# Kernel tuning notes

Hardware: AMD Instinct MI355X
Metric: run time of the kernel (lower is better)

The kernel has to match this reference:

```python
import jax, jax.numpy as jnp
import numpy as np

N = 20000          # nodes
F = 256            # num_node_features (== num_sampled_vectors)
FEAT_EMB = 63      # feat_emb_dim
EMB = FEAT_EMB + 1 # emb_dim = feat_emb_dim + val_emb_dim
CH = F * EMB       # 16384, conv1 input channels
HID = 128
OUT = 7
E = 320000         # edges


def setup_inputs() -> dict:
    key = jax.random.key(0)
    ks = jax.random.split(key, 7)
    x = jax.random.normal(ks[0], (N, F), dtype=jnp.float32)
    emb_table = jax.random.normal(ks[1], (F, FEAT_EMB), dtype=jnp.float32) * 0.02
    W1 = jax.random.normal(ks[2], (CH, HID), dtype=jnp.float32) / np.sqrt(CH)
    b1 = jnp.zeros((HID,), jnp.float32)
    W2 = jax.random.normal(ks[3], (HID, OUT), dtype=jnp.float32) / np.sqrt(HID)
    b2 = jnp.zeros((OUT,), jnp.float32)
    edge_index = jax.random.randint(ks[4], (2, E), 0, N, dtype=jnp.int32)
    return {"x": x, "emb_table": emb_table, "W1": W1, "b1": b1,
            "W2": W2, "b2": b2, "edge_index": edge_index}


def _gcn_conv(h, W, b, src, dst, norm, n):
    # PyG GCNConv: symmetric-normalized aggregation (with self loops) of x @ W, then + bias
    h = h @ W                                   # [n, out]
    msg = h[src] * norm[:, None]                # gather + edge-weight
    agg = jax.ops.segment_sum(msg, dst, num_segments=n)  # scatter-add
    return agg + b


def reference(x, emb_table, W1, b1, W2, b2, edge_index):
    n = x.shape[0]
    # StandardScaler: per-feature zero mean, unit (population) std
    mean = x.mean(axis=0)
    std = x.std(axis=0)
    std = jnp.where(std == 0, jnp.float32(1.0), std)
    xs = (x - mean) / std                       # [n, F]
    # feature embedding construction: per node, concat emb_table with its value column
    feats = jnp.concatenate(
        [jnp.broadcast_to(emb_table[None], (n, F, FEAT_EMB)), xs[:, :, None]],
        axis=-1,
    ).reshape(n, CH)                            # [n, F*EMB]
    # GCN normalization with self loops (eval mode: no dropout_adj / dropout)
    loop = jnp.arange(n, dtype=edge_index.dtype)
    src = jnp.concatenate([edge_index[0], loop])
    dst = jnp.concatenate([edge_index[1], loop])
    deg = jax.ops.segment_sum(jnp.ones_like(src, jnp.float32), dst, num_segments=n)
    dinv = jnp.where(deg > 0, jax.lax.rsqrt(deg), jnp.float32(0.0))
    norm = dinv[src] * dinv[dst]                # [E+n]
    h = jax.nn.relu(_gcn_conv(feats, W1, b1, src, dst, norm, n))
    out = _gcn_conv(h, W2, b2, src, dst, norm, n)
    return jax.nn.log_softmax(out, axis=1)
```

## Files before the change

### kernel.cpp

```cpp
#include <hip/hip_runtime.h>
#include <math.h>

#define F_   256
#define FEAT_EMB_ 63
#define HID_ 128
#define OUT_ 7
#define SLOTS 64
#define NP 16

typedef short short8 __attribute__((ext_vector_type(8)));
typedef float f32x4 __attribute__((ext_vector_type(4)));

__device__ inline short f2bf(float f) {
    unsigned u = __float_as_uint(f);
    u += 0x7FFFu + ((u >> 16) & 1u);
    return (short)(u >> 16);
}

#define K1_CS 625
#define K1_ED 625
#define K1_CV 256
#define K1_PK 16
#define K1_GRID (K1_CS + K1_ED + K1_CV + K1_PK)

__global__ __launch_bounds__(256) void k1_kernel(const float* __restrict__ x,
                                                 const int* __restrict__ ei,
                                                 const float* __restrict__ emb,
                                                 const float* __restrict__ W1,
                                                 float* __restrict__ colsum16,
                                                 float* __restrict__ colsq16,
                                                 int* __restrict__ deg,
                                                 int* __restrict__ adjP,
                                                 float* __restrict__ Cp16,
                                                 short* __restrict__ Wfrag, int E) {
    __shared__ float4 smem[8 * 64];
    int b = blockIdx.x;
    int t = threadIdx.x;

    if (b < K1_CS) {
        int rl = t >> 6, lane = t & 63;
        int row0 = b * 32 + rl * 8;
        float4 v[8];
#pragma unroll
        for (int i = 0; i < 8; i++)
            v[i] = *(const float4*)(x + (size_t)(row0 + i) * F_ + lane * 4);
        float4 s = make_float4(0.f, 0.f, 0.f, 0.f);
        float4 q = make_float4(0.f, 0.f, 0.f, 0.f);
#pragma unroll
        for (int i = 0; i < 8; i++) {
            s.x += v[i].x; s.y += v[i].y; s.z += v[i].z; s.w += v[i].w;
            q.x += v[i].x * v[i].x; q.y += v[i].y * v[i].y;
            q.z += v[i].z * v[i].z; q.w += v[i].w * v[i].w;
        }
        smem[rl * 64 + lane] = s;
        smem[(rl + 4) * 64 + lane] = q;
        __syncthreads();
        if (rl == 0) {
#pragma unroll
            for (int i = 1; i < 4; i++) {
                float4 a = smem[i * 64 + lane], bq = smem[(i + 4) * 64 + lane];
                s.x += a.x; s.y += a.y; s.z += a.z; s.w += a.w;
                q.x += bq.x; q.y += bq.y; q.z += bq.z; q.w += bq.w;
            }
            int buf = (b & (NP - 1)) * F_;
            atomicAdd(&colsum16[buf + lane * 4 + 0], s.x);
            atomicAdd(&colsum16[buf + lane * 4 + 1], s.y);
            atomicAdd(&colsum16[buf + lane * 4 + 2], s.z);
            atomicAdd(&colsum16[buf + lane * 4 + 3], s.w);
            atomicAdd(&colsq16[buf + lane * 4 + 0], q.x);
            atomicAdd(&colsq16[buf + lane * 4 + 1], q.y);
            atomicAdd(&colsq16[buf + lane * 4 + 2], q.z);
            atomicAdd(&colsq16[buf + lane * 4 + 3], q.w);
        }
    } else if (b < K1_CS + K1_ED) {
        int e0 = (b - K1_CS) * 512 + t;
#pragma unroll
        for (int i = 0; i < 2; i++) {
            int e = e0 + i * 256;
            if (e < E) {
                int s = ei[e];
                int d = ei[E + e];
                int pos = atomicAdd(&deg[d], 1);
                if (pos < SLOTS) adjP[(d << 6) + pos] = s;
            }
        }
    } else if (b < K1_CS + K1_ED + K1_CV) {
        int f = b - (K1_CS + K1_ED);
        int jg = t >> 5, k4 = t & 31;
        float4 s = make_float4(0.f, 0.f, 0.f, 0.f);
        for (int j = jg; j < FEAT_EMB_; j += 8) {
            float e = emb[f * FEAT_EMB_ + j];
            float4 w = *(const float4*)(W1 + ((size_t)(f * 64 + j)) * HID_ + k4 * 4);
            s.x += e * w.x; s.y += e * w.y; s.z += e * w.z; s.w += e * w.w;
        }
        smem[jg * 32 + k4] = s;
        __syncthreads();
        if (jg == 0) {
#pragma unroll
            for (int i = 1; i < 8; i++) {
                float4 a = smem[i * 32 + k4];
                s.x += a.x; s.y += a.y; s.z += a.z; s.w += a.w;
            }
            int buf = (f & (NP - 1)) * HID_;
            atomicAdd(&Cp16[buf + k4 * 4 + 0], s.x);
            atomicAdd(&Cp16[buf + k4 * 4 + 1], s.y);
            atomicAdd(&Cp16[buf + k4 * 4 + 2], s.z);
            atomicAdd(&Cp16[buf + k4 * 4 + 3], s.w);
        }
    } else {
        int pb = b - (K1_CS + K1_ED + K1_CV);
        int f0 = pb * 16;
#pragma unroll
        for (int i = 0; i < 8; i++) {
            int idx = t + i * 256;
            int f = f0 + (idx >> 7);
            int nn = idx & 127;
            float w = W1[((size_t)(f * 64 + 63)) * HID_ + nn];
            int kc = f >> 5, j = f & 7, hi2 = (f >> 3) & 3;
            int lane = hi2 * 16 + (nn & 15);
            int nt = nn >> 4;
            Wfrag[(((kc * 8 + nt) * 64 + lane) << 3) + j] = f2bf(w);
        }
    }
}

__global__ __launch_bounds__(256) void mm1_kernel(const float* __restrict__ x,
                                                  const short* __restrict__ Wfrag,
                                                  const float* __restrict__ Cp16,
                                                  const float* __restrict__ colsum16,
                                                  const float* __restrict__ colsq16,
                                                  const int* __restrict__ deg,
                                                  unsigned short* __restrict__ g0b,
                                                  int n) {
    __shared__ float cps[HID_];
    __shared__ float smean[F_];
    __shared__ float srstd[F_];
    int t = threadIdx.x;
    {
        float s = 0.f, q = 0.f;
#pragma unroll
        for (int p = 0; p < NP; p++) {
            s += colsum16[p * F_ + t];
            q += colsq16[p * F_ + t];
        }
        float m = s / (float)n;
        float var = fmaxf(q / (float)n - m * m, 0.f);
        float sd = sqrtf(var);
        smean[t] = m;
        srstd[t] = (sd == 0.f) ? 1.f : (1.f / sd);
    }
    if (t < HID_) {
        float s = 0.f;
#pragma unroll
        for (int p = 0; p < NP; p++) s += Cp16[p * HID_ + t];
        cps[t] = s;
    }
    __syncthreads();

    int wave = t >> 6, lane = t & 63;
    int m = lane & 15;
    int hi = lane >> 4;
    int rowbase = blockIdx.x * 64 + wave * 16;
    int arow = rowbase + m;
    bool rok = arow < n;
    const float* xrow = x + (size_t)arow * F_ + hi * 8;

    float4 xa[8], xb[8];
    if (rok) {
#pragma unroll
        for (int kc = 0; kc < 8; kc++) {
            xa[kc] = *(const float4*)(xrow + kc * 32);
            xb[kc] = *(const float4*)(xrow + kc * 32 + 4);
        }
    }

    const float4* smv = (const float4*)smean;
    const float4* srv = (const float4*)srstd;

    f32x4 acc[8];
#pragma unroll
    for (int i = 0; i < 8; i++) acc[i] = (f32x4){0.f, 0.f, 0.f, 0.f};

#pragma unroll
    for (int kc = 0; kc < 8; kc++) {
        short8 af;
        if (rok) {
            int mb = kc * 8 + hi * 2;
            float4 m0 = smv[mb], m1 = smv[mb + 1];
            float4 r0 = srv[mb], r1 = srv[mb + 1];
            af[0] = f2bf((xa[kc].x - m0.x) * r0.x);
            af[1] = f2bf((xa[kc].y - m0.y) * r0.y);
            af[2] = f2bf((xa[kc].z - m0.z) * r0.z);
            af[3] = f2bf((xa[kc].w - m0.w) * r0.w);
            af[4] = f2bf((xb[kc].x - m1.x) * r1.x);
            af[5] = f2bf((xb[kc].y - m1.y) * r1.y);
            af[6] = f2bf((xb[kc].z - m1.z) * r1.z);
            af[7] = f2bf((xb[kc].w - m1.w) * r1.w);
        } else {
            af = (short8){0, 0, 0, 0, 0, 0, 0, 0};
        }
#pragma unroll
        for (int nt = 0; nt < 8; nt++) {
            short8 bf = *(const short8*)(Wfrag + (((kc * 8 + nt) * 64 + lane) << 3));
            acc[nt] = __builtin_amdgcn_mfma_f32_16x16x32_bf16(af, bf, acc[nt], 0, 0, 0);
        }
    }

    float dv[4];
#pragma unroll
    for (int r = 0; r < 4; r++) {
        int gr = rowbase + hi * 4 + r;
        dv[r] = (gr < n) ? rsqrtf((float)deg[gr] + 1.0f) : 0.f;
    }
#pragma unroll
    for (int nt = 0; nt < 8; nt++) {
        int col = nt * 16 + m;
        float cp = cps[col];
#pragma unroll
        for (int r = 0; r < 4; r++) {
            int gr = rowbase + hi * 4 + r;
            if (gr < n)
                g0b[(size_t)gr * HID_ + col] = (unsigned short)f2bf((acc[nt][r] + cp) * dv[r]);
        }
    }
}

__global__ __launch_bounds__(256) void agg_fc2_kernel(const unsigned short* __restrict__ g0b,
                                                      const int* __restrict__ deg,
                                                      const int* __restrict__ adjP,
                                                      const float* __restrict__ b1,
                                                      const float* __restrict__ W2,
                                                      float* __restrict__ g2, int n) {
    int wave = threadIdx.x >> 6;
    int lane = threadIdx.x & 63;
    int d = blockIdx.x * 4 + wave;
    if (d >= n) return;

    int dgv = deg[d];
    int o0 = d << 6;
    int o1 = o0 + min(dgv, SLOTS);
    unsigned u = *(const unsigned*)(g0b + (size_t)d * HID_ + lane * 2);
    float ax = __uint_as_float(u << 16);
    float ay = __uint_as_float(u & 0xFFFF0000u);

    for (int base = o0; base < o1; base += 64) {
        int idx = (base + lane < o1) ? adjP[base + lane] : 0;
        int c2 = min(64, o1 - base);
        int j = 0;
        for (; j + 4 <= c2; j += 4) {
            int s0 = __shfl(idx, j + 0);
            int s1 = __shfl(idx, j + 1);
            int s2 = __shfl(idx, j + 2);
            int s3 = __shfl(idx, j + 3);
            unsigned u0 = *(const unsigned*)(g0b + (size_t)s0 * HID_ + lane * 2);
            unsigned u1 = *(const unsigned*)(g0b + (size_t)s1 * HID_ + lane * 2);
            unsigned u2 = *(const unsigned*)(g0b + (size_t)s2 * HID_ + lane * 2);
            unsigned u3 = *(const unsigned*)(g0b + (size_t)s3 * HID_ + lane * 2);
            ax += __uint_as_float(u0 << 16) + __uint_as_float(u1 << 16)
                + __uint_as_float(u2 << 16) + __uint_as_float(u3 << 16);
            ay += __uint_as_float(u0 & 0xFFFF0000u) + __uint_as_float(u1 & 0xFFFF0000u)
                + __uint_as_float(u2 & 0xFFFF0000u) + __uint_as_float(u3 & 0xFFFF0000u);
        }
        for (; j < c2; j++) {
            int s = __shfl(idx, j);
            unsigned uu = *(const unsigned*)(g0b + (size_t)s * HID_ + lane * 2);
            ax += __uint_as_float(uu << 16);
            ay += __uint_as_float(uu & 0xFFFF0000u);
        }
    }

    float dv = rsqrtf((float)dgv + 1.0f);
    float2 bb = *(const float2*)(b1 + lane * 2);
    float h0 = fmaxf(ax * dv + bb.x, 0.f);
    float h1 = fmaxf(ay * dv + bb.y, 0.f);

    const float* w2a = W2 + (lane * 2) * OUT_;
    const float* w2b = W2 + (lane * 2 + 1) * OUT_;
    float r[OUT_];
#pragma unroll
    for (int c = 0; c < OUT_; c++) {
        float p = h0 * w2a[c] + h1 * w2b[c];
#pragma unroll
        for (int off = 32; off > 0; off >>= 1) p += __shfl_xor(p, off);
        r[c] = p;
    }
    if (lane < 8) {
        float val;
        switch (lane) {
            case 0: val = r[0]; break;
            case 1: val = r[1]; break;
            case 2: val = r[2]; break;
            case 3: val = r[3]; break;
            case 4: val = r[4]; break;
            case 5: val = r[5]; break;
            case 6: val = r[6]; break;
            default: val = 0.f; break;
        }
        g2[(size_t)d * 8 + lane] = val * dv;
    }
}

__global__ __launch_bounds__(256) void agg2_softmax_kernel(const float* __restrict__ g2,
                                                           const int* __restrict__ deg,
                                                           const int* __restrict__ adjP,
                                                           const float* __restrict__ b2,
                                                           float* __restrict__ out, int n) {
    int t = threadIdx.x;
    int g = t >> 3;
    int c = t & 7;
    int d = blockIdx.x * 32 + g;
    if (d >= n) return;

    int dgv = deg[d];
    int o0 = d << 6;
    int o1 = o0 + min(dgv, SLOTS);
    float acc = g2[(size_t)d * 8 + c];
    int i = o0;
    for (; i + 2 <= o1; i += 2) {
        int s0 = adjP[i], s1 = adjP[i + 1];
        acc += g2[(size_t)s0 * 8 + c] + g2[(size_t)s1 * 8 + c];
    }
    for (; i < o1; i++) acc += g2[(size_t)adjP[i] * 8 + c];

    float dv = rsqrtf((float)dgv + 1.0f);
    float z = (c < OUT_) ? (acc * dv + b2[c]) : -INFINITY;
    float m = z;
#pragma unroll
    for (int off = 4; off > 0; off >>= 1) m = fmaxf(m, __shfl_xor(m, off, 8));
    float e = (c < OUT_) ? __expf(z - m) : 0.f;
    float sum = e;
#pragma unroll
    for (int off = 4; off > 0; off >>= 1) sum += __shfl_xor(sum, off, 8);
    if (c < OUT_) out[(size_t)d * OUT_ + c] = z - m - __logf(sum);
}

extern "C" void kernel_launch(void* const* d_in, const int* in_sizes, int n_in,
                              void* d_out, int out_size, void* d_ws, size_t ws_size,
                              hipStream_t stream) {
    const float* x    = (const float*)d_in[0];
    const float* emb  = (const float*)d_in[1];
    const float* W1   = (const float*)d_in[2];
    const float* b1   = (const float*)d_in[3];
    const float* W2   = (const float*)d_in[4];
    const float* b2   = (const float*)d_in[5];
    const int*   ei   = (const int*)d_in[6];
    float* out = (float*)d_out;

    const int N = in_sizes[0] / F_;
    const int E = in_sizes[6] / 2;

    float* ws = (float*)d_ws;
    size_t o = 0;
    float* colsum16 = ws + o; o += NP * F_;
    float* colsq16  = ws + o; o += NP * F_;
    float* Cp16     = ws + o; o += NP * HID_;
    int*   deg      = (int*)(ws + o); o += N;
    size_t zero_elems = o;
    short* Wfrag    = (short*)(ws + o); o += (size_t)F_ * HID_ / 2;
    int*   adjP     = (int*)(ws + o); o += (size_t)N * SLOTS;
    unsigned short* g0b = (unsigned short*)(ws + o); o += (size_t)N * HID_ / 2;
    float* g2       = ws + o; o += (size_t)N * 8;

    hipMemsetAsync(ws, 0, zero_elems * sizeof(float), stream);
    k1_kernel<<<K1_GRID, 256, 0, stream>>>(x, ei, emb, W1, colsum16, colsq16,
                                           deg, adjP, Cp16, Wfrag, E);
    mm1_kernel<<<(N + 63) / 64, 256, 0, stream>>>(x, Wfrag, Cp16, colsum16, colsq16,
                                                  deg, g0b, N);
    agg_fc2_kernel<<<(N + 3) / 4, 256, 0, stream>>>(g0b, deg, adjP, b1, W2, g2, N);
    agg2_softmax_kernel<<<(N + 31) / 32, 256, 0, stream>>>(g2, deg, adjP, b2, out, N);
}
```

Baseline: 147.7 us.

## Fold standardization into W1 fragments in shared memory, widen aggregation loops

The per-feature mean and std scaling moves into the weight side. Each mm1 block now builds a bf16 W1 fragment scaled by rstd in LDS (64KB) and adds a bias correction of -mean*w into the constant term. This removes the separate packing blocks in k1 and the per-element normalization of x, at the cost of every mm1 block reading and converting the W1 value columns redundantly. It also raises occupancy pressure from the larger LDS footprint. Separately, the first aggregation unrolls its gather by 8 instead of 4, and the second aggregation splits each node's neighbour list across two half-groups that are combined with a shuffle.

```diff
diff --git a/kernel.cpp b/kernel.cpp
--- a/kernel.cpp
+++ b/kernel.cpp
@@ -20,8 +20,7 @@
 #define K1_CS 625
 #define K1_ED 625
 #define K1_CV 256
-#define K1_PK 16
-#define K1_GRID (K1_CS + K1_ED + K1_CV + K1_PK)
+#define K1_GRID (K1_CS + K1_ED + K1_CV)
 
 __global__ __launch_bounds__(256) void k1_kernel(const float* __restrict__ x,
                                                  const int* __restrict__ ei,
@@ -32,7 +31,7 @@
                                                  int* __restrict__ deg,
                                                  int* __restrict__ adjP,
                                                  float* __restrict__ Cp16,
-                                                 short* __restrict__ Wfrag, int E) {
+                                                 int E) {
     __shared__ float4 smem[8 * 64];
     int b = blockIdx.x;
     int t = threadIdx.x;
@@ -84,7 +83,7 @@
                 if (pos < SLOTS) adjP[(d << 6) + pos] = s;
             }
         }
-    } else if (b < K1_CS + K1_ED + K1_CV) {
+    } else {
         int f = b - (K1_CS + K1_ED);
         int jg = t >> 5, k4 = t & 31;
         float4 s = make_float4(0.f, 0.f, 0.f, 0.f);
@@ -107,35 +106,23 @@
             atomicAdd(&Cp16[buf + k4 * 4 + 2], s.z);
             atomicAdd(&Cp16[buf + k4 * 4 + 3], s.w);
         }
-    } else {
-        int pb = b - (K1_CS + K1_ED + K1_CV);
-        int f0 = pb * 16;
-#pragma unroll
-        for (int i = 0; i < 8; i++) {
-            int idx = t + i * 256;
-            int f = f0 + (idx >> 7);
-            int nn = idx & 127;
-            float w = W1[((size_t)(f * 64 + 63)) * HID_ + nn];
-            int kc = f >> 5, j = f & 7, hi2 = (f >> 3) & 3;
-            int lane = hi2 * 16 + (nn & 15);
-            int nt = nn >> 4;
-            Wfrag[(((kc * 8 + nt) * 64 + lane) << 3) + j] = f2bf(w);
-        }
     }
 }
 
 __global__ __launch_bounds__(256) void mm1_kernel(const float* __restrict__ x,
-                                                  const short* __restrict__ Wfrag,
-                                                  const float* __restrict__ Cp16,
+                                                  const float* __restrict__ W1,
                                                   const float* __restrict__ colsum16,
                                                   const float* __restrict__ colsq16,
+                                                  const float* __restrict__ Cp16,
                                                   const int* __restrict__ deg,
                                                   unsigned short* __restrict__ g0b,
                                                   int n) {
+    __shared__ short wfrag[F_ * HID_];
+    __shared__ float smean[F_], srstd[F_];
+    __shared__ float red[256];
     __shared__ float cps[HID_];
-    __shared__ float smean[F_];
-    __shared__ float srstd[F_];
     int t = threadIdx.x;
+
     {
         float s = 0.f, q = 0.f;
 #pragma unroll
@@ -149,11 +136,31 @@
         smean[t] = m;
         srstd[t] = (sd == 0.f) ? 1.f : (1.f / sd);
     }
+    __syncthreads();
+
+    {
+        int nn = t & 127;
+        int f0 = t >> 7;
+        float cacc = 0.f;
+#pragma unroll
+        for (int i = 0; i < 128; i++) {
+            int f = f0 + i * 2;
+            float w = W1[((size_t)(f * 64 + 63)) * HID_ + nn];
+            float wr = w * srstd[f];
+            cacc -= smean[f] * wr;
+            int kc = f >> 5, j = f & 7, hi2 = (f >> 3) & 3;
+            int lane = hi2 * 16 + (nn & 15);
+            int nt = nn >> 4;
+            wfrag[(((kc * 8 + nt) * 64 + lane) << 3) + j] = f2bf(wr);
+        }
+        red[t] = cacc;
+    }
+    __syncthreads();
     if (t < HID_) {
-        float s = 0.f;
-#pragma unroll
-        for (int p = 0; p < NP; p++) s += Cp16[p * HID_ + t];
-        cps[t] = s;
+        float cv = 0.f;
+#pragma unroll
+        for (int p = 0; p < NP; p++) cv += Cp16[p * HID_ + t];
+        cps[t] = cv + red[t] + red[t + 128];
     }
     __syncthreads();
 
@@ -165,17 +172,26 @@
     bool rok = arow < n;
     const float* xrow = x + (size_t)arow * F_ + hi * 8;
 
-    float4 xa[8], xb[8];
+    short8 af[8];
     if (rok) {
+        float4 xa[8], xb[8];
 #pragma unroll
         for (int kc = 0; kc < 8; kc++) {
             xa[kc] = *(const float4*)(xrow + kc * 32);
             xb[kc] = *(const float4*)(xrow + kc * 32 + 4);
         }
-    }
-
-    const float4* smv = (const float4*)smean;
-    const float4* srv = (const float4*)srstd;
+#pragma unroll
+        for (int kc = 0; kc < 8; kc++) {
+            af[kc][0] = f2bf(xa[kc].x); af[kc][1] = f2bf(xa[kc].y);
+            af[kc][2] = f2bf(xa[kc].z); af[kc][3] = f2bf(xa[kc].w);
+            af[kc][4] = f2bf(xb[kc].x); af[kc][5] = f2bf(xb[kc].y);
+            af[kc][6] = f2bf(xb[kc].z); af[kc][7] = f2bf(xb[kc].w);
+        }
+    } else {
+#pragma unroll
+        for (int kc = 0; kc < 8; kc++)
+            af[kc] = (short8){0, 0, 0, 0, 0, 0, 0, 0};
+    }
 
     f32x4 acc[8];
 #pragma unroll
@@ -183,26 +199,10 @@
 
 #pragma unroll
     for (int kc = 0; kc < 8; kc++) {
-        short8 af;
-        if (rok) {
-            int mb = kc * 8 + hi * 2;
-            float4 m0 = smv[mb], m1 = smv[mb + 1];
-            float4 r0 = srv[mb], r1 = srv[mb + 1];
-            af[0] = f2bf((xa[kc].x - m0.x) * r0.x);
-            af[1] = f2bf((xa[kc].y - m0.y) * r0.y);
-            af[2] = f2bf((xa[kc].z - m0.z) * r0.z);
-            af[3] = f2bf((xa[kc].w - m0.w) * r0.w);
-            af[4] = f2bf((xb[kc].x - m1.x) * r1.x);
-            af[5] = f2bf((xb[kc].y - m1.y) * r1.y);
-            af[6] = f2bf((xb[kc].z - m1.z) * r1.z);
-            af[7] = f2bf((xb[kc].w - m1.w) * r1.w);
-        } else {
-            af = (short8){0, 0, 0, 0, 0, 0, 0, 0};
-        }
 #pragma unroll
         for (int nt = 0; nt < 8; nt++) {
-            short8 bf = *(const short8*)(Wfrag + (((kc * 8 + nt) * 64 + lane) << 3));
-            acc[nt] = __builtin_amdgcn_mfma_f32_16x16x32_bf16(af, bf, acc[nt], 0, 0, 0);
+            short8 bf = *(const short8*)(wfrag + (((kc * 8 + nt) * 64 + lane) << 3));
+            acc[nt] = __builtin_amdgcn_mfma_f32_16x16x32_bf16(af[kc], bf, acc[nt], 0, 0, 0);
         }
     }
 
@@ -247,19 +247,18 @@
         int idx = (base + lane < o1) ? adjP[base + lane] : 0;
         int c2 = min(64, o1 - base);
         int j = 0;
-        for (; j + 4 <= c2; j += 4) {
-            int s0 = __shfl(idx, j + 0);
-            int s1 = __shfl(idx, j + 1);
-            int s2 = __shfl(idx, j + 2);
-            int s3 = __shfl(idx, j + 3);
-            unsigned u0 = *(const unsigned*)(g0b + (size_t)s0 * HID_ + lane * 2);
-            unsigned u1 = *(const unsigned*)(g0b + (size_t)s1 * HID_ + lane * 2);
-            unsigned u2 = *(const unsigned*)(g0b + (size_t)s2 * HID_ + lane * 2);
-            unsigned u3 = *(const unsigned*)(g0b + (size_t)s3 * HID_ + lane * 2);
-            ax += __uint_as_float(u0 << 16) + __uint_as_float(u1 << 16)
-                + __uint_as_float(u2 << 16) + __uint_as_float(u3 << 16);
-            ay += __uint_as_float(u0 & 0xFFFF0000u) + __uint_as_float(u1 & 0xFFFF0000u)
-                + __uint_as_float(u2 & 0xFFFF0000u) + __uint_as_float(u3 & 0xFFFF0000u);
+        for (; j + 8 <= c2; j += 8) {
+            unsigned uu[8];
+#pragma unroll
+            for (int k = 0; k < 8; k++) {
+                int s = __shfl(idx, j + k);
+                uu[k] = *(const unsigned*)(g0b + (size_t)s * HID_ + lane * 2);
+            }
+#pragma unroll
+            for (int k = 0; k < 8; k++) {
+                ax += __uint_as_float(uu[k] << 16);
+                ay += __uint_as_float(uu[k] & 0xFFFF0000u);
+            }
         }
         for (; j < c2; j++) {
             int s = __shfl(idx, j);
@@ -306,28 +305,26 @@
                                                            const float* __restrict__ b2,
                                                            float* __restrict__ out, int n) {
     int t = threadIdx.x;
-    int g = t >> 3;
-    int c = t & 7;
-    int d = blockIdx.x * 32 + g;
+    int g = t >> 4;
+    int c = t & 15;
+    int ch = c & 7, half = c >> 3;
+    int d = blockIdx.x * 16 + g;
     if (d >= n) return;
 
     int dgv = deg[d];
     int o0 = d << 6;
     int o1 = o0 + min(dgv, SLOTS);
-    float acc = g2[(size_t)d * 8 + c];
-    int i = o0;
-    for (; i + 2 <= o1; i += 2) {
-        int s0 = adjP[i], s1 = adjP[i + 1];
-        acc += g2[(size_t)s0 * 8 + c] + g2[(size_t)s1 * 8 + c];
-    }
-    for (; i < o1; i++) acc += g2[(size_t)adjP[i] * 8 + c];
+    float acc = (half == 0) ? g2[(size_t)d * 8 + ch] : 0.f;
+    for (int i = o0 + half; i < o1; i += 2)
+        acc += g2[(size_t)adjP[i] * 8 + ch];
+    acc += __shfl_xor(acc, 8, 16);
 
     float dv = rsqrtf((float)dgv + 1.0f);
-    float z = (c < OUT_) ? (acc * dv + b2[c]) : -INFINITY;
+    float z = (ch < OUT_) ? (acc * dv + b2[ch]) : -INFINITY;
     float m = z;
 #pragma unroll
     for (int off = 4; off > 0; off >>= 1) m = fmaxf(m, __shfl_xor(m, off, 8));
-    float e = (c < OUT_) ? __expf(z - m) : 0.f;
+    float e = (ch < OUT_) ? __expf(z - m) : 0.f;
     float sum = e;
 #pragma unroll
     for (int off = 4; off > 0; off >>= 1) sum += __shfl_xor(sum, off, 8);
@@ -356,16 +353,15 @@
     float* Cp16     = ws + o; o += NP * HID_;
     int*   deg      = (int*)(ws + o); o += N;
     size_t zero_elems = o;
-    short* Wfrag    = (short*)(ws + o); o += (size_t)F_ * HID_ / 2;
     int*   adjP     = (int*)(ws + o); o += (size_t)N * SLOTS;
     unsigned short* g0b = (unsigned short*)(ws + o); o += (size_t)N * HID_ / 2;
     float* g2       = ws + o; o += (size_t)N * 8;
 
     hipMemsetAsync(ws, 0, zero_elems * sizeof(float), stream);
     k1_kernel<<<K1_GRID, 256, 0, stream>>>(x, ei, emb, W1, colsum16, colsq16,
-                                           deg, adjP, Cp16, Wfrag, E);
-    mm1_kernel<<<(N + 63) / 64, 256, 0, stream>>>(x, Wfrag, Cp16, colsum16, colsq16,
+                                           deg, adjP, Cp16, E);
+    mm1_kernel<<<(N + 63) / 64, 256, 0, stream>>>(x, W1, colsum16, colsq16, Cp16,
                                                   deg, g0b, N);
     agg_fc2_kernel<<<(N + 3) / 4, 256, 0, stream>>>(g0b, deg, adjP, b1, W2, g2, N);
-    agg2_softmax_kernel<<<(N + 31) / 32, 256, 0, stream>>>(g2, deg, adjP, b2, out, N);
-}
+    agg2_softmax_kernel<<<(N + 15) / 16, 256, 0, stream>>>(g2, deg, adjP, b2, out, N);
+}
```

New measurement: 148.3 us. Within noise of the previous version (+0.4%).
